# Performance work log

Hardware: AMD Instinct MI355X
Metric: run time of the kernel (lower is better)

Reference implementation:

```python
import jax, jax.numpy as jnp
import numpy as np

WIN = 9
EPS = 1e-05


def _box3d(x, win=WIN):
    """Sum over a win^3 box (zero-padded), equivalent to conv3d with a ones kernel.
    Implemented as three separable 1D convolutions (exact same math, O(win)/voxel)."""
    pad = win // 2
    for axis in range(3):  # spatial axes D, H, W
        kshape = [1, 1, 1, 1, 1]
        kshape[2 + axis] = win
        kern = jnp.ones(kshape, x.dtype)
        pads = [(0, 0)] * 3
        pads[axis] = (pad, pad)
        dn = jax.lax.conv_dimension_numbers(x.shape, kern.shape, ('NCDHW', 'OIDHW', 'NCDHW'))
        x = jax.lax.conv_general_dilated(x, kern, window_strides=(1, 1, 1),
                                         padding=pads, dimension_numbers=dn)
    return x


def setup_inputs() -> dict:
    key = jax.random.key(0)
    k1, k2 = jax.random.split(key)
    shape = (1, 1, 160, 192, 224)  # [N, C, D, H, W] brain-MRI-scale volume
    I = jax.random.normal(k1, shape, dtype=jnp.float32)
    J = jax.random.normal(k2, shape, dtype=jnp.float32)
    return {"I": I, "J": J}


def reference(I, J):
    win_size = WIN ** 3
    I2 = I * I
    J2 = J * J
    IJ = I * J
    I_sum = _box3d(I)
    J_sum = _box3d(J)
    I2_sum = _box3d(I2)
    J2_sum = _box3d(J2)
    IJ_sum = _box3d(IJ)
    u_I = I_sum / win_size
    u_J = J_sum / win_size
    cross = IJ_sum - u_J * I_sum - u_I * J_sum + u_I * u_J * win_size
    I_var = I2_sum - 2 * u_I * I_sum + u_I * u_I * win_size
    J_var = J2_sum - 2 * u_J * J_sum + u_J * u_J * win_size
    cc = cross * cross / (I_var * J_var + EPS)
    return -1.0 * jnp.mean(cc)
```

## Files before the change

kernel.cpp:

```cpp
#include <hip/hip_runtime.h>


#define DD 160
#define HH 192
#define WW 224
#define W4 56
#define SLICE (HH * WW)
#define S4 (SLICE / 4)
#define NVOX (DD * SLICE)
#define TW 32
#define TH 16
#define DCH 10
#define NTHR 512
#define SW_RS 36
#define SW_CS (24 * SW_RS)
#define SH_RS 33
#define SH_CS (TH * SH_RS)
#define EPS 1e-5f
#define INV_WSUM (1.0f / 729.0f)

__global__ __launch_bounds__(NTHR, 4) void ncc_fused(const float* __restrict__ I,
                                                     const float* __restrict__ J,
                                                     float* __restrict__ out) {
    __shared__ float SW0[5 * SW_CS], SW1[5 * SW_CS];
    __shared__ float SH0[5 * SH_CS], SH1[5 * SH_CS];
    __shared__ float wred[NTHR / 64];

    const int tid = threadIdx.x;
    const int tx = tid & 31, ty = tid >> 5;
    const int wlo = blockIdx.x * TW;
    const int hlo = blockIdx.y * TH;
    const int dlo = blockIdx.z * DCH;

    const int wr = tid >> 3, wc = tid & 7;
    const int gh = hlo - 4 + wr;
    const bool hok = (gh >= 0) && (gh < HH);
    const int gf0 = (wlo >> 2) - 1 + wc;

    const int ht = tid - 192;
    const int hcol = ht & 31, hch = ht >> 5;

    const float4* Iv = (const float4*)I;
    const float4* Jv = (const float4*)J;

    auto w_stage = [&](int z, float* dst) {
        const int rowb = z * S4 + gh * W4;
        float ax[12], bx[12];
        #pragma unroll
        for (int k = 0; k < 3; ++k) {
            const int f = gf0 + k;
            float4 a = make_float4(0.f, 0.f, 0.f, 0.f);
            float4 b = make_float4(0.f, 0.f, 0.f, 0.f);
            if (hok && f >= 0 && f < W4) { a = Iv[rowb + f]; b = Jv[rowb + f]; }
            ax[4*k] = a.x; ax[4*k+1] = a.y; ax[4*k+2] = a.z; ax[4*k+3] = a.w;
            bx[4*k] = b.x; bx[4*k+1] = b.y; bx[4*k+2] = b.z; bx[4*k+3] = b.w;
        }
        float* wp = dst + wr * SW_RS + 4 * wc;
        #pragma unroll
        for (int ch = 0; ch < 5; ++ch) {
            float v[12];
            #pragma unroll
            for (int k = 0; k < 12; ++k)
                v[k] = (ch == 0) ? ax[k]
                     : (ch == 1) ? bx[k]
                     : (ch == 2) ? ax[k] * ax[k]
                     : (ch == 3) ? bx[k] * bx[k]
                     :             ax[k] * bx[k];
            float s = v[0];
            #pragma unroll
            for (int k = 1; k < 9; ++k) s += v[k];
            float4 o;
            o.x = s;
            s += v[9]  - v[0]; o.y = s;
            s += v[10] - v[1]; o.z = s;
            s += v[11] - v[2]; o.w = s;
            *(float4*)(wp + ch * SW_CS) = o;
        }
    };

    float q0[9], q1[9], q2[9], q3[9], q4[9];
    #pragma unroll
    for (int k = 0; k < 9; ++k) { q0[k]=0.f; q1[k]=0.f; q2[k]=0.f; q3[k]=0.f; q4[k]=0.f; }
    float r0=0.f, r1=0.f, r2=0.f, r3=0.f, r4=0.f;
    float acc = 0.f;

    {
        const int z0 = dlo - 4;
        if (tid < 192 && z0 >= 0) w_stage(z0, SW0);
    }
    __syncthreads();

    #pragma unroll 1
    for (int g = 0; g < 2; ++g) {
        #pragma unroll
        for (int ph = 0; ph < 9; ++ph) {
            const int i = g * 9 + ph;
            const int z = dlo - 4 + i;
            const bool val = (z >= 0) && (z < DD);
            const int par = (g + ph) & 1;
            float* swR = par ? SW1 : SW0;
            float* swW = par ? SW0 : SW1;
            float* sh  = par ? SH1 : SH0;

            if (tid < 192) {
                const int zn = z + 1;
                if (i < DCH + 7 && zn >= 0 && zn < DD) w_stage(zn, swW);
            } else if (ht < 160 && val) {
                const float* p = swR + hch * SW_CS + hcol;
                float v[24];
                #pragma unroll
                for (int r = 0; r < 24; ++r) v[r] = p[r * SW_RS];
                float s = v[0];
                #pragma unroll
                for (int r = 1; r < 9; ++r) s += v[r];
                float* o = sh + hch * SH_CS + hcol;
                o[0] = s;
                #pragma unroll
                for (int r = 1; r < 16; ++r) {
                    s += v[r + 8] - v[r - 1];
                    o[r * SH_RS] = s;
                }
            }
            __syncthreads();

            float w0=0.f, w1=0.f, w2=0.f, w3=0.f, w4=0.f;
            if (val) {
                const float* p = sh + ty * SH_RS + tx;
                w0 = p[0];
                w1 = p[SH_CS];
                w2 = p[2 * SH_CS];
                w3 = p[3 * SH_CS];
                w4 = p[4 * SH_CS];
            }
            r0 += w0 - q0[ph]; q0[ph] = w0;
            r1 += w1 - q1[ph]; q1[ph] = w1;
            r2 += w2 - q2[ph]; q2[ph] = w2;
            r3 += w3 - q3[ph]; q3[ph] = w3;
            r4 += w4 - q4[ph]; q4[ph] = w4;

            if (i >= 8) {
                float cross = r4 - r0 * r1 * INV_WSUM;
                float iv    = r2 - r0 * r0 * INV_WSUM;
                float jv    = r3 - r1 * r1 * INV_WSUM;
                acc += cross * cross * __builtin_amdgcn_rcpf(iv * jv + EPS);
            }
        }
    }

    #pragma unroll
    for (int off = 32; off > 0; off >>= 1) acc += __shfl_down(acc, off, 64);
    if ((tid & 63) == 0) wred[tid >> 6] = acc;
    __syncthreads();
    if (tid == 0) {
        float t = 0.f;
        #pragma unroll
        for (int k = 0; k < NTHR / 64; ++k) t += wred[k];
        atomicAdd(out, t * (-1.0f / (float)NVOX));
    }
}

extern "C" void kernel_launch(void* const* d_in, const int* in_sizes, int n_in,
                              void* d_out, int out_size, void* d_ws, size_t ws_size,
                              hipStream_t stream) {
    const float* I = (const float*)d_in[0];
    const float* J = (const float*)d_in[1];
    float* out = (float*)d_out;

    hipMemsetAsync(d_out, 0, sizeof(float), stream);

    dim3 blk(NTHR, 1, 1);
    dim3 grd(WW / TW, HH / TH, DD / DCH);
    ncc_fused<<<grd, blk, 0, stream>>>(I, J, out);
}
```

Baseline: 140.6 us.

## Double depth chunk per block, single-buffer H-stage LDS, raise occupancy bound

Each block now covers 20 depth slices instead of 10, which cuts the redundant 8-slice halo recomputation along D. The loop runs a fixed 36 iterations, with the tail ones masked out. The double-buffered H-pass LDS is replaced by one buffer in a channel-interleaved layout. That frees LDS and adds a second barrier per iteration. The launch-bounds occupancy hint goes from 4 to 6. The trade-off is half as many blocks, which worsens tail balance, plus extra barriers and 8 idle iterations per block.

```diff
diff --git a/kernel.cpp b/kernel.cpp
--- a/kernel.cpp
+++ b/kernel.cpp
@@ -10,20 +10,19 @@
 #define NVOX (DD * SLICE)
 #define TW 32
 #define TH 16
-#define DCH 10
+#define DCH 20
+#define ITERS (DCH + 8)
 #define NTHR 512
 #define SW_RS 36
 #define SW_CS (24 * SW_RS)
-#define SH_RS 33
-#define SH_CS (TH * SH_RS)
 #define EPS 1e-5f
 #define INV_WSUM (1.0f / 729.0f)
 
-__global__ __launch_bounds__(NTHR, 4) void ncc_fused(const float* __restrict__ I,
+__global__ __launch_bounds__(NTHR, 6) void ncc_fused(const float* __restrict__ I,
                                                      const float* __restrict__ J,
                                                      float* __restrict__ out) {
     __shared__ float SW0[5 * SW_CS], SW1[5 * SW_CS];
-    __shared__ float SH0[5 * SH_CS], SH1[5 * SH_CS];
+    __shared__ float SH[TH * TW * 5];
     __shared__ float wred[NTHR / 64];
 
     const int tid = threadIdx.x;
@@ -84,53 +83,51 @@
     float r0=0.f, r1=0.f, r2=0.f, r3=0.f, r4=0.f;
     float acc = 0.f;
 
-    {
-        const int z0 = dlo - 4;
-        if (tid < 192 && z0 >= 0) w_stage(z0, SW0);
-    }
+    if (tid < 192 && dlo >= 4) w_stage(dlo - 4, SW0);
     __syncthreads();
 
     #pragma unroll 1
-    for (int g = 0; g < 2; ++g) {
+    for (int g = 0; g < 4; ++g) {
         #pragma unroll
         for (int ph = 0; ph < 9; ++ph) {
-            const int i = g * 9 + ph;
+            const int i = 9 * g + ph;
             const int z = dlo - 4 + i;
-            const bool val = (z >= 0) && (z < DD);
-            const int par = (g + ph) & 1;
+            const bool live = (i < ITERS);
+            const bool val = live && (z >= 0) && (z < DD);
+            const int par = i & 1;
             float* swR = par ? SW1 : SW0;
             float* swW = par ? SW0 : SW1;
-            float* sh  = par ? SH1 : SH0;
 
             if (tid < 192) {
                 const int zn = z + 1;
-                if (i < DCH + 7 && zn >= 0 && zn < DD) w_stage(zn, swW);
+                if (i < ITERS - 1 && zn >= 0 && zn < DD) w_stage(zn, swW);
             } else if (ht < 160 && val) {
                 const float* p = swR + hch * SW_CS + hcol;
                 float v[24];
                 #pragma unroll
-                for (int r = 0; r < 24; ++r) v[r] = p[r * SW_RS];
+                for (int r = 0; r < 24; r += 2) {
+                    const float* pr = p + r * SW_RS;
+                    v[r]     = pr[0];
+                    v[r + 1] = pr[SW_RS];
+                }
                 float s = v[0];
                 #pragma unroll
                 for (int r = 1; r < 9; ++r) s += v[r];
-                float* o = sh + hch * SH_CS + hcol;
+                float* o = SH + hcol * 5 + hch;
+                float prev = s;
                 o[0] = s;
                 #pragma unroll
                 for (int r = 1; r < 16; ++r) {
-                    s += v[r + 8] - v[r - 1];
-                    o[r * SH_RS] = s;
+                    prev += v[r + 8] - v[r - 1];
+                    o[r * (TW * 5)] = prev;
                 }
             }
             __syncthreads();
 
             float w0=0.f, w1=0.f, w2=0.f, w3=0.f, w4=0.f;
             if (val) {
-                const float* p = sh + ty * SH_RS + tx;
-                w0 = p[0];
-                w1 = p[SH_CS];
-                w2 = p[2 * SH_CS];
-                w3 = p[3 * SH_CS];
-                w4 = p[4 * SH_CS];
+                const float* p = SH + (ty * TW + tx) * 5;
+                w0 = p[0]; w1 = p[1]; w2 = p[2]; w3 = p[3]; w4 = p[4];
             }
             r0 += w0 - q0[ph]; q0[ph] = w0;
             r1 += w1 - q1[ph]; q1[ph] = w1;
@@ -138,12 +135,13 @@
             r3 += w3 - q3[ph]; q3[ph] = w3;
             r4 += w4 - q4[ph]; q4[ph] = w4;
 
-            if (i >= 8) {
+            if (live && i >= 8) {
                 float cross = r4 - r0 * r1 * INV_WSUM;
                 float iv    = r2 - r0 * r0 * INV_WSUM;
                 float jv    = r3 - r1 * r1 * INV_WSUM;
                 acc += cross * cross * __builtin_amdgcn_rcpf(iv * jv + EPS);
             }
+            __syncthreads();
         }
     }
 
```

New measurement: 204.8 us. 1.46x slower.
